# Optimization experiments

Hardware: AMD Instinct MI355X
Metric: run time of the kernel (lower is better)

## Reference

```python
import jax, jax.numpy as jnp
import numpy as np


def setup_inputs() -> dict:
    key = jax.random.key(0)
    ks = jax.random.split(key, 8)
    S, B, I, H, O = 2048, 64, 256, 512, 512
    s = 0.05  # small weight scale for numerical stability over long scans
    return {
        "x": jax.random.normal(ks[0], (S, B, I), dtype=jnp.float32),
        "Wi": jax.random.normal(ks[1], (H, I + H), dtype=jnp.float32) * s,
        "bi": jnp.zeros((H,), dtype=jnp.float32),
        "Wf": jax.random.normal(ks[2], (H, I + H), dtype=jnp.float32) * s,
        "bf": jnp.zeros((H,), dtype=jnp.float32),
        "Wg": jax.random.normal(ks[3], (H, I + H), dtype=jnp.float32) * s,
        "bg": jnp.zeros((H,), dtype=jnp.float32),
        "Wo": jax.random.normal(ks[4], (H, I + H), dtype=jnp.float32) * s,
        "bo": jnp.zeros((H,), dtype=jnp.float32),
        "Wh2o": jax.random.normal(ks[5], (O, H), dtype=jnp.float32) * s,
        "bh2o": jnp.zeros((O,), dtype=jnp.float32),
    }


def reference(x, Wi, bi, Wf, bf, Wg, bg, Wo, bo, Wh2o, bh2o):
    # x: [S, B, I] seq-major. Returns log-softmax outputs [S, B, O].
    S, B, I = x.shape
    H = Wi.shape[0]
    h0 = jnp.zeros((B, H), dtype=x.dtype)
    c0 = jnp.zeros((B, H), dtype=x.dtype)

    def step(carry, xt):
        h, c = carry
        comb = jnp.concatenate([xt, h], axis=1)  # [B, I+H]
        i = jax.nn.sigmoid(comb @ Wi.T + bi)
        f = jax.nn.sigmoid(comb @ Wf.T + bf)
        g = jnp.tanh(comb @ Wg.T + bg)
        o = jax.nn.sigmoid(comb @ Wo.T + bo)
        c_new = f * c + i * g
        h_new = o * jnp.tanh(c_new)
        out = jax.nn.log_softmax(h_new @ Wh2o.T + bh2o, axis=-1)
        return (h_new, c_new), out

    (_, _), outs = jax.lax.scan(step, (h0, c0), x)
    return outs  # [S, B, O]
```

## Files before the change

kernel.cpp:

```cpp
#include <hip/hip_runtime.h>
#include <hip/hip_bf16.h>

typedef __attribute__((ext_vector_type(8))) short bf16x8;
typedef __attribute__((ext_vector_type(4))) float f32x4;
typedef unsigned int u32t;

#define S_LEN 2048
#define BATCH 64
#define IDIM 256
#define HDIM 512
#define KDIM 768
#define ODIM 512
#define NGRP 4
#define NSLOT 32
#define LDK 792
#define FLAG_PAD 16
#define POLL_CAP 10000

#define OFF_PRE (16 * LDK * 2)
#define OFF_BIAS (OFF_PRE + 2 * 4 * 16 * 17 * 4)
#define SMEM_BYTES 98304

__device__ __forceinline__ unsigned short f2b(float f) {
  __hip_bfloat16 h = __float2bfloat16(f);
  return __builtin_bit_cast(unsigned short, h);
}
__device__ __forceinline__ float sigmoidf_(float x) { return 1.0f / (1.0f + __expf(-x)); }
__device__ __forceinline__ float tanhf_(float x) { return 1.0f - 2.0f / (1.0f + __expf(2.0f * x)); }

__device__ __forceinline__ bf16x8 cvt8(float4 v0, float4 v1) {
  bf16x8 b;
  b[0] = (short)f2b(v0.x); b[1] = (short)f2b(v0.y);
  b[2] = (short)f2b(v0.z); b[3] = (short)f2b(v0.w);
  b[4] = (short)f2b(v1.x); b[5] = (short)f2b(v1.y);
  b[6] = (short)f2b(v1.z); b[7] = (short)f2b(v1.w);
  return b;
}

__device__ __forceinline__ int l2_flag_read(int* p) {
  int z = 0;
  asm volatile("" : "+v"(z));
  return __hip_atomic_fetch_add(p, z, __ATOMIC_RELAXED, __HIP_MEMORY_SCOPE_WORKGROUP);
}

__global__ void lstm_init(const float* __restrict__ wh2o,
                          __hip_bfloat16* __restrict__ wh2o_bf,
                          __hip_bfloat16* __restrict__ h_all,
                          int* __restrict__ ctrl) {
  int idx = blockIdx.x * 256 + threadIdx.x;
  if (idx < ODIM * HDIM) wh2o_bf[idx] = __float2bfloat16(wh2o[idx]);
  if (idx < BATCH * HDIM) h_all[idx] = __float2bfloat16(0.0f);
  if (idx < 4096) ctrl[idx] = 0;
}

__global__ __launch_bounds__(512) void lstm_recur(
    const float* __restrict__ x,
    const float* __restrict__ Wi, const float* __restrict__ bi,
    const float* __restrict__ Wf, const float* __restrict__ bfp,
    const float* __restrict__ Wg, const float* __restrict__ bgp,
    const float* __restrict__ Wo, const float* __restrict__ bop,
    __hip_bfloat16* __restrict__ h_all, int* __restrict__ flags,
    int* __restrict__ cnt) {
  extern __shared__ char smem[];
  __shared__ int sel[2];
  const int tid = threadIdx.x;
  const int lane = tid & 63;
  const int wave = tid >> 6;

  if (tid == 0) {
    unsigned xcd;
    asm("s_getreg_b32 %0, hwreg(HW_REG_XCC_ID)" : "=s"(xcd));
    sel[0] = (int)(xcd & 7);
    sel[1] = atomicAdd(&cnt[(xcd & 7) * 16], 1);
  }
  __syncthreads();
  const int g = sel[0];
  const int s = sel[1];
  if (g >= NGRP || s >= NSLOT) return;

  short* comb = (short*)smem;
  float* pre = (float*)(smem + OFF_PRE);
  float* blds = (float*)(smem + OFF_BIAS);

  const int ct = wave & 3;
  const int kh = wave >> 2;
  const int rc16 = lane & 15;
  const int ksub = (lane >> 4) * 8;

  const float* wsrc = (ct == 0) ? Wi : (ct == 1) ? Wf : (ct == 2) ? Wg : Wo;
  const float* wrow = wsrc + (size_t)(s * 16 + rc16) * KDIM;
  bf16x8 bfx[4], bfh[8];
#pragma unroll
  for (int kk = 0; kk < 4; ++kk) {
    int k0 = kh * 128 + kk * 32 + ksub;
    bfx[kk] = cvt8(*(const float4*)(wrow + k0), *(const float4*)(wrow + k0 + 4));
  }
#pragma unroll
  for (int kk = 0; kk < 8; ++kk) {
    int k0 = IDIM + kh * 256 + kk * 32 + ksub;
    bfh[kk] = cvt8(*(const float4*)(wrow + k0), *(const float4*)(wrow + k0 + 4));
  }
  if (tid < 64) {
    int gate = tid >> 4;
    const float* bsrc = (gate == 0) ? bi : (gate == 1) ? bfp : (gate == 2) ? bgp : bop;
    blds[tid] = bsrc[s * 16 + (tid & 15)];
  }

  float4 rx[2];
  auto ldx = [&](int t) {
    const float4* xs = (const float4*)(x + ((size_t)t * BATCH + g * 16) * IDIM);
    rx[0] = xs[tid];
    rx[1] = xs[tid + 512];
  };
  auto stx = [&]() {
#pragma unroll
    for (int j = 0; j < 2; ++j) {
      int i = tid + j * 512;
      int r = i >> 6, k4 = i & 63;
      float4 v = rx[j];
      ushort4 u;
      u.x = f2b(v.x); u.y = f2b(v.y); u.z = f2b(v.z); u.w = f2b(v.w);
      *(ushort4*)&comb[r * LDK + k4 * 4] = u;
    }
  };

  const short* acx = &comb[rc16 * LDK + kh * 128 + ksub];
  const short* ach = &comb[rc16 * LDK + IDIM + kh * 256 + ksub];

  ldx(0);
  stx();
  __syncthreads();
  f32x4 acc = {}, acc2 = {};
  acc = __builtin_amdgcn_mfma_f32_16x16x32_bf16(*(const bf16x8*)(acx + 0), bfx[0], acc, 0, 0, 0);
  acc2 = __builtin_amdgcn_mfma_f32_16x16x32_bf16(*(const bf16x8*)(acx + 32), bfx[1], acc2, 0, 0, 0);
  acc = __builtin_amdgcn_mfma_f32_16x16x32_bf16(*(const bf16x8*)(acx + 64), bfx[2], acc, 0, 0, 0);
  acc2 = __builtin_amdgcn_mfma_f32_16x16x32_bf16(*(const bf16x8*)(acx + 96), bfx[3], acc2, 0, 0, 0);
  ldx(1);

  float cst = 0.0f;
  const int gm = tid >> 4;
  const int gn = tid & 15;
  int* myflag = flags + (g * NSLOT + s) * FLAG_PAD;
  int* gflags = flags + g * NSLOT * FLAG_PAD;

  for (int t = 0; t < S_LEN; ++t) {
    if (wave == 0) {
      for (int it = 0; it < POLL_CAP; ++it) {
        int v = (lane < NSLOT) ? l2_flag_read(gflags + lane * FLAG_PAD) : 0x7fffffff;
        if (__all(v >= t)) break;
        __builtin_amdgcn_s_sleep(1);
      }
    }
    __syncthreads();
    {
      const short* hs = (const short*)h_all + ((size_t)t * BATCH + g * 16) * HDIM;
      int r = tid >> 5, c16 = tid & 31;
      const short* sp = hs + r * HDIM + c16 * 16;
      bf16x8 v0 = *(const bf16x8*)sp;
      bf16x8 v1 = *(const bf16x8*)(sp + 8);
      short* dp = &comb[r * LDK + IDIM + c16 * 16];
      *(bf16x8*)dp = v0;
      *(bf16x8*)(dp + 8) = v1;
    }
    __syncthreads();
#pragma unroll
    for (int kk = 0; kk < 8; kk += 2) {
      acc = __builtin_amdgcn_mfma_f32_16x16x32_bf16(*(const bf16x8*)(ach + kk * 32), bfh[kk],
                                                    acc, 0, 0, 0);
      acc2 = __builtin_amdgcn_mfma_f32_16x16x32_bf16(*(const bf16x8*)(ach + kk * 32 + 32),
                                                     bfh[kk + 1], acc2, 0, 0, 0);
    }
#pragma unroll
    for (int j = 0; j < 4; ++j) {
      int m = (lane >> 4) * 4 + j;
      pre[((kh * 4 + ct) * 16 + m) * 17 + rc16] = acc[j] + acc2[j];
    }
    __syncthreads();
    if (tid < 256) {
      float pi = blds[gn] + pre[(0 * 16 + gm) * 17 + gn] + pre[(4 * 16 + gm) * 17 + gn];
      float pf = blds[16 + gn] + pre[(1 * 16 + gm) * 17 + gn] + pre[(5 * 16 + gm) * 17 + gn];
      float pg = blds[32 + gn] + pre[(2 * 16 + gm) * 17 + gn] + pre[(6 * 16 + gm) * 17 + gn];
      float po = blds[48 + gn] + pre[(3 * 16 + gm) * 17 + gn] + pre[(7 * 16 + gm) * 17 + gn];
      float ig = sigmoidf_(pi), fg = sigmoidf_(pf), gv = tanhf_(pg), og = sigmoidf_(po);
      cst = fg * cst + ig * gv;
      float hv = og * tanhf_(cst);
      float hv2 = __shfl_xor(hv, 1);
      if ((gn & 1) == 0) {
        u32t hw = (u32t)f2b(hv) | ((u32t)f2b(hv2) << 16);
        u32t* dst = (u32t*)((short*)h_all +
                            ((size_t)(t + 1) * BATCH + g * 16 + gm) * HDIM + s * 16 + gn);
        *dst = hw;
      }
    }
    asm volatile("s_waitcnt vmcnt(0)" ::: "memory");
    __syncthreads();
    if (tid == 0)
      __hip_atomic_store(myflag, t + 1, __ATOMIC_RELAXED, __HIP_MEMORY_SCOPE_WORKGROUP);
    if (t + 1 < S_LEN) {
      stx();
      __syncthreads();
      f32x4 z = {};
      acc = z;
      acc2 = z;
      acc = __builtin_amdgcn_mfma_f32_16x16x32_bf16(*(const bf16x8*)(acx + 0), bfx[0], acc, 0, 0, 0);
      acc2 = __builtin_amdgcn_mfma_f32_16x16x32_bf16(*(const bf16x8*)(acx + 32), bfx[1], acc2, 0, 0, 0);
      acc = __builtin_amdgcn_mfma_f32_16x16x32_bf16(*(const bf16x8*)(acx + 64), bfx[2], acc, 0, 0, 0);
      acc2 = __builtin_amdgcn_mfma_f32_16x16x32_bf16(*(const bf16x8*)(acx + 96), bfx[3], acc2, 0, 0, 0);
      ldx((t + 2 < S_LEN) ? t + 2 : S_LEN - 1);
    }
  }
}

__global__ __launch_bounds__(256) void lstm_out(
    const __hip_bfloat16* __restrict__ h_all,
    const __hip_bfloat16* __restrict__ wh2o_bf, const float* __restrict__ bh2o,
    float* __restrict__ out) {
  const int t = blockIdx.x;
  const int tid = threadIdx.x;
  const int lane = tid & 63;
  const int wave = tid >> 6;
  const int r0 = wave * 16;
  const short* abase = (const short*)h_all +
                       ((size_t)(t + 1) * BATCH + r0 + (lane & 15)) * HDIM + (lane >> 4) * 8;
  const short* bbase = (const short*)wh2o_bf + (size_t)(lane & 15) * HDIM + (lane >> 4) * 8;
  f32x4 acc[32];
  f32x4 zero = {0.f, 0.f, 0.f, 0.f};
#pragma unroll
  for (int n = 0; n < 32; ++n) acc[n] = zero;
  for (int kk = 0; kk < 16; ++kk) {
    bf16x8 a = *(const bf16x8*)(abase + kk * 32);
#pragma unroll
    for (int n = 0; n < 32; ++n) {
      bf16x8 b = *(const bf16x8*)(bbase + (size_t)n * 16 * HDIM + kk * 32);
      acc[n] = __builtin_amdgcn_mfma_f32_16x16x32_bf16(a, b, acc[n], 0, 0, 0);
    }
  }
  float mx[4] = {-3.0e38f, -3.0e38f, -3.0e38f, -3.0e38f};
#pragma unroll
  for (int n = 0; n < 32; ++n) {
    float bn = bh2o[n * 16 + (lane & 15)];
#pragma unroll
    for (int j = 0; j < 4; ++j) {
      acc[n][j] += bn;
      mx[j] = fmaxf(mx[j], acc[n][j]);
    }
  }
#pragma unroll
  for (int j = 0; j < 4; ++j) {
    mx[j] = fmaxf(mx[j], __shfl_xor(mx[j], 1));
    mx[j] = fmaxf(mx[j], __shfl_xor(mx[j], 2));
    mx[j] = fmaxf(mx[j], __shfl_xor(mx[j], 4));
    mx[j] = fmaxf(mx[j], __shfl_xor(mx[j], 8));
  }
  float sm[4] = {0.f, 0.f, 0.f, 0.f};
#pragma unroll
  for (int n = 0; n < 32; ++n) {
#pragma unroll
    for (int j = 0; j < 4; ++j) sm[j] += __expf(acc[n][j] - mx[j]);
  }
#pragma unroll
  for (int j = 0; j < 4; ++j) {
    sm[j] += __shfl_xor(sm[j], 1);
    sm[j] += __shfl_xor(sm[j], 2);
    sm[j] += __shfl_xor(sm[j], 4);
    sm[j] += __shfl_xor(sm[j], 8);
  }
  float ls[4];
#pragma unroll
  for (int j = 0; j < 4; ++j) ls[j] = mx[j] + __logf(sm[j]);
  float* ob = out + (size_t)t * BATCH * ODIM;
#pragma unroll
  for (int n = 0; n < 32; ++n) {
#pragma unroll
    for (int j = 0; j < 4; ++j) {
      int row = r0 + (lane >> 4) * 4 + j;
      ob[(size_t)row * ODIM + n * 16 + (lane & 15)] = acc[n][j] - ls[j];
    }
  }
}

extern "C" void kernel_launch(void* const* d_in, const int* in_sizes, int n_in,
                              void* d_out, int out_size, void* d_ws, size_t ws_size,
                              hipStream_t stream) {
  const float* x = (const float*)d_in[0];
  const float* Wi = (const float*)d_in[1];
  const float* bi = (const float*)d_in[2];
  const float* Wf = (const float*)d_in[3];
  const float* bf = (const float*)d_in[4];
  const float* Wg = (const float*)d_in[5];
  const float* bg = (const float*)d_in[6];
  const float* Wo = (const float*)d_in[7];
  const float* bo = (const float*)d_in[8];
  const float* Wh2o = (const float*)d_in[9];
  const float* bh2o = (const float*)d_in[10];

  char* ws = (char*)d_ws;
  int* cnt = (int*)ws;
  int* flags = (int*)(ws + 4096);
  __hip_bfloat16* h_all = (__hip_bfloat16*)(ws + 16384);
  size_t h_all_b = (size_t)(S_LEN + 1) * BATCH * HDIM * 2;
  __hip_bfloat16* wh2o_bf = (__hip_bfloat16*)(ws + 16384 + h_all_b);
  size_t needed = 16384 + h_all_b + (size_t)ODIM * HDIM * 2;
  if (ws_size < needed || n_in < 11) return;

  hipFuncSetAttribute((const void*)lstm_recur,
                      hipFuncAttributeMaxDynamicSharedMemorySize, SMEM_BYTES);

  lstm_init<<<1024, 256, 0, stream>>>(Wh2o, wh2o_bf, h_all, (int*)ws);
  lstm_recur<<<256, 512, SMEM_BYTES, stream>>>(x, Wi, bi, Wf, bf, Wg, bg, Wo, bo,
                                               h_all, flags, cnt);
  lstm_out<<<S_LEN, 256, 0, stream>>>(h_all, wh2o_bf, bh2o, (float*)d_out);
}
```

Before: 11.46 ms.

## Halve slots per group, use arrival-counter epoch barrier, double-buffer x slab

New measurement: 20.86 ms. 81.9% more time.

```diff
diff --git a/kernel.cpp b/kernel.cpp
--- a/kernel.cpp
+++ b/kernel.cpp
@@ -12,13 +12,16 @@
 #define KDIM 768
 #define ODIM 512
 #define NGRP 4
-#define NSLOT 32
-#define LDK 792
-#define FLAG_PAD 16
-#define POLL_CAP 10000
-
-#define OFF_PRE (16 * LDK * 2)
-#define OFF_BIAS (OFF_PRE + 2 * 4 * 16 * 17 * 4)
+#define NSLOT 16
+#define LDX 264
+#define LDH 520
+#define XSLAB (16 * LDX)
+#define EP_PAD 32
+#define POLL_CAP (1 << 16)
+
+#define OFF_H 16896
+#define OFF_PRE 33536
+#define OFF_BIAS 41984
 #define SMEM_BYTES 98304
 
 __device__ __forceinline__ unsigned short f2b(float f) {
@@ -37,7 +40,7 @@
   return b;
 }
 
-__device__ __forceinline__ int l2_flag_read(int* p) {
+__device__ __forceinline__ int l2_read(int* p) {
   int z = 0;
   asm volatile("" : "+v"(z));
   return __hip_atomic_fetch_add(p, z, __ATOMIC_RELAXED, __HIP_MEMORY_SCOPE_WORKGROUP);
@@ -50,7 +53,7 @@
   int idx = blockIdx.x * 256 + threadIdx.x;
   if (idx < ODIM * HDIM) wh2o_bf[idx] = __float2bfloat16(wh2o[idx]);
   if (idx < BATCH * HDIM) h_all[idx] = __float2bfloat16(0.0f);
-  if (idx < 4096) ctrl[idx] = 0;
+  if (idx < 16384) ctrl[idx] = 0;
 }
 
 __global__ __launch_bounds__(512) void lstm_recur(
@@ -59,8 +62,8 @@
     const float* __restrict__ Wf, const float* __restrict__ bfp,
     const float* __restrict__ Wg, const float* __restrict__ bgp,
     const float* __restrict__ Wo, const float* __restrict__ bop,
-    __hip_bfloat16* __restrict__ h_all, int* __restrict__ flags,
-    int* __restrict__ cnt) {
+    __hip_bfloat16* __restrict__ h_all, int* __restrict__ epoch,
+    int* __restrict__ stepcnt, int* __restrict__ cnt) {
   extern __shared__ char smem[];
   __shared__ int sel[2];
   const int tid = threadIdx.x;
@@ -78,32 +81,33 @@
   const int s = sel[1];
   if (g >= NGRP || s >= NSLOT) return;
 
-  short* comb = (short*)smem;
+  short* xsl = (short*)smem;
+  short* hsl = (short*)(smem + OFF_H);
   float* pre = (float*)(smem + OFF_PRE);
   float* blds = (float*)(smem + OFF_BIAS);
 
   const int ct = wave & 3;
-  const int kh = wave >> 2;
-  const int rc16 = lane & 15;
+  const int ch = wave >> 2;
+  const int a_r = lane & 15;
   const int ksub = (lane >> 4) * 8;
 
   const float* wsrc = (ct == 0) ? Wi : (ct == 1) ? Wf : (ct == 2) ? Wg : Wo;
-  const float* wrow = wsrc + (size_t)(s * 16 + rc16) * KDIM;
-  bf16x8 bfx[4], bfh[8];
-#pragma unroll
-  for (int kk = 0; kk < 4; ++kk) {
-    int k0 = kh * 128 + kk * 32 + ksub;
+  const float* wrow = wsrc + (size_t)(s * 32 + ch * 16 + a_r) * KDIM;
+  bf16x8 bfx[8], bfh[16];
+#pragma unroll
+  for (int kk = 0; kk < 8; ++kk) {
+    int k0 = kk * 32 + ksub;
     bfx[kk] = cvt8(*(const float4*)(wrow + k0), *(const float4*)(wrow + k0 + 4));
   }
 #pragma unroll
-  for (int kk = 0; kk < 8; ++kk) {
-    int k0 = IDIM + kh * 256 + kk * 32 + ksub;
+  for (int kk = 0; kk < 16; ++kk) {
+    int k0 = IDIM + kk * 32 + ksub;
     bfh[kk] = cvt8(*(const float4*)(wrow + k0), *(const float4*)(wrow + k0 + 4));
   }
-  if (tid < 64) {
-    int gate = tid >> 4;
+  if (tid < 128) {
+    int gate = tid >> 5;
     const float* bsrc = (gate == 0) ? bi : (gate == 1) ? bfp : (gate == 2) ? bgp : bop;
-    blds[tid] = bsrc[s * 16 + (tid & 15)];
+    blds[tid] = bsrc[s * 32 + (tid & 31)];
   }
 
   float4 rx[2];
@@ -112,7 +116,7 @@
     rx[0] = xs[tid];
     rx[1] = xs[tid + 512];
   };
-  auto stx = [&]() {
+  auto stx = [&](int par) {
 #pragma unroll
     for (int j = 0; j < 2; ++j) {
       int i = tid + j * 512;
@@ -120,94 +124,93 @@
       float4 v = rx[j];
       ushort4 u;
       u.x = f2b(v.x); u.y = f2b(v.y); u.z = f2b(v.z); u.w = f2b(v.w);
-      *(ushort4*)&comb[r * LDK + k4 * 4] = u;
+      *(ushort4*)&xsl[par * XSLAB + r * LDX + k4 * 4] = u;
     }
   };
 
-  const short* acx = &comb[rc16 * LDK + kh * 128 + ksub];
-  const short* ach = &comb[rc16 * LDK + IDIM + kh * 256 + ksub];
-
   ldx(0);
-  stx();
-  __syncthreads();
-  f32x4 acc = {}, acc2 = {};
-  acc = __builtin_amdgcn_mfma_f32_16x16x32_bf16(*(const bf16x8*)(acx + 0), bfx[0], acc, 0, 0, 0);
-  acc2 = __builtin_amdgcn_mfma_f32_16x16x32_bf16(*(const bf16x8*)(acx + 32), bfx[1], acc2, 0, 0, 0);
-  acc = __builtin_amdgcn_mfma_f32_16x16x32_bf16(*(const bf16x8*)(acx + 64), bfx[2], acc, 0, 0, 0);
-  acc2 = __builtin_amdgcn_mfma_f32_16x16x32_bf16(*(const bf16x8*)(acx + 96), bfx[3], acc2, 0, 0, 0);
+  stx(0);
   ldx(1);
 
   float cst = 0.0f;
-  const int gm = tid >> 4;
-  const int gn = tid & 15;
-  int* myflag = flags + (g * NSLOT + s) * FLAG_PAD;
-  int* gflags = flags + g * NSLOT * FLAG_PAD;
+  const int gr = tid >> 5;
+  const int gc = tid & 31;
+  int* myep = epoch + (g * NSLOT + s) * EP_PAD;
+  int* gep = epoch + g * NSLOT * EP_PAD;
+  int* gstep = stepcnt + g * S_LEN;
 
   for (int t = 0; t < S_LEN; ++t) {
     if (wave == 0) {
+      int old = 0;
+      if (lane == 0)
+        old = __hip_atomic_fetch_add(&gstep[t], 1, __ATOMIC_RELAXED,
+                                     __HIP_MEMORY_SCOPE_WORKGROUP);
+      old = __shfl(old, 0);
+      if (old == NSLOT - 1 && lane < NSLOT)
+        __hip_atomic_store(gep + lane * EP_PAD, t, __ATOMIC_RELAXED,
+                           __HIP_MEMORY_SCOPE_WORKGROUP);
       for (int it = 0; it < POLL_CAP; ++it) {
-        int v = (lane < NSLOT) ? l2_flag_read(gflags + lane * FLAG_PAD) : 0x7fffffff;
-        if (__all(v >= t)) break;
+        if (l2_read(myep) >= t) break;
         __builtin_amdgcn_s_sleep(1);
       }
     }
     __syncthreads();
+    stx((t + 1) & 1);
     {
       const short* hs = (const short*)h_all + ((size_t)t * BATCH + g * 16) * HDIM;
       int r = tid >> 5, c16 = tid & 31;
       const short* sp = hs + r * HDIM + c16 * 16;
       bf16x8 v0 = *(const bf16x8*)sp;
       bf16x8 v1 = *(const bf16x8*)(sp + 8);
-      short* dp = &comb[r * LDK + IDIM + c16 * 16];
+      short* dp = &hsl[r * LDH + c16 * 16];
       *(bf16x8*)dp = v0;
       *(bf16x8*)(dp + 8) = v1;
     }
+    ldx((t + 2 < S_LEN) ? t + 2 : S_LEN - 1);
     __syncthreads();
-#pragma unroll
-    for (int kk = 0; kk < 8; kk += 2) {
-      acc = __builtin_amdgcn_mfma_f32_16x16x32_bf16(*(const bf16x8*)(ach + kk * 32), bfh[kk],
-                                                    acc, 0, 0, 0);
-      acc2 = __builtin_amdgcn_mfma_f32_16x16x32_bf16(*(const bf16x8*)(ach + kk * 32 + 32),
-                                                     bfh[kk + 1], acc2, 0, 0, 0);
-    }
-#pragma unroll
-    for (int j = 0; j < 4; ++j) {
-      int m = (lane >> 4) * 4 + j;
-      pre[((kh * 4 + ct) * 16 + m) * 17 + rc16] = acc[j] + acc2[j];
+    {
+      const short* acx = &xsl[(t & 1) * XSLAB + a_r * LDX + ksub];
+      const short* ach = &hsl[a_r * LDH + ksub];
+      f32x4 c0 = {}, c1 = {}, c2 = {}, c3 = {};
+#pragma unroll
+      for (int kk = 0; kk < 8; kk += 2) {
+        c0 = __builtin_amdgcn_mfma_f32_16x16x32_bf16(*(const bf16x8*)(acx + kk * 32),
+                                                     bfx[kk], c0, 0, 0, 0);
+        c1 = __builtin_amdgcn_mfma_f32_16x16x32_bf16(*(const bf16x8*)(acx + kk * 32 + 32),
+                                                     bfx[kk + 1], c1, 0, 0, 0);
+      }
+#pragma unroll
+      for (int kk = 0; kk < 16; kk += 2) {
+        c2 = __builtin_amdgcn_mfma_f32_16x16x32_bf16(*(const bf16x8*)(ach + kk * 32),
+                                                     bfh[kk], c2, 0, 0, 0);
+        c3 = __builtin_amdgcn_mfma_f32_16x16x32_bf16(*(const bf16x8*)(ach + kk * 32 + 32),
+                                                     bfh[kk + 1], c3, 0, 0, 0);
+      }
+      const int rb = (lane >> 4) * 4;
+      const int col = ch * 16 + a_r;
+#pragma unroll
+      for (int j = 0; j < 4; ++j)
+        pre[(ct * 16 + rb + j) * 33 + col] = c0[j] + c1[j] + c2[j] + c3[j];
     }
     __syncthreads();
-    if (tid < 256) {
-      float pi = blds[gn] + pre[(0 * 16 + gm) * 17 + gn] + pre[(4 * 16 + gm) * 17 + gn];
-      float pf = blds[16 + gn] + pre[(1 * 16 + gm) * 17 + gn] + pre[(5 * 16 + gm) * 17 + gn];
-      float pg = blds[32 + gn] + pre[(2 * 16 + gm) * 17 + gn] + pre[(6 * 16 + gm) * 17 + gn];
-      float po = blds[48 + gn] + pre[(3 * 16 + gm) * 17 + gn] + pre[(7 * 16 + gm) * 17 + gn];
+    {
+      float pi = blds[gc] + pre[(0 * 16 + gr) * 33 + gc];
+      float pf = blds[32 + gc] + pre[(1 * 16 + gr) * 33 + gc];
+      float pg = blds[64 + gc] + pre[(2 * 16 + gr) * 33 + gc];
+      float po = blds[96 + gc] + pre[(3 * 16 + gr) * 33 + gc];
       float ig = sigmoidf_(pi), fg = sigmoidf_(pf), gv = tanhf_(pg), og = sigmoidf_(po);
       cst = fg * cst + ig * gv;
       float hv = og * tanhf_(cst);
       float hv2 = __shfl_xor(hv, 1);
-      if ((gn & 1) == 0) {
+      if (!(gc & 1)) {
         u32t hw = (u32t)f2b(hv) | ((u32t)f2b(hv2) << 16);
         u32t* dst = (u32t*)((short*)h_all +
-                            ((size_t)(t + 1) * BATCH + g * 16 + gm) * HDIM + s * 16 + gn);
+                            ((size_t)(t + 1) * BATCH + g * 16 + gr) * HDIM + s * 32 + gc);
         *dst = hw;
       }
     }
     asm volatile("s_waitcnt vmcnt(0)" ::: "memory");
     __syncthreads();
-    if (tid == 0)
-      __hip_atomic_store(myflag, t + 1, __ATOMIC_RELAXED, __HIP_MEMORY_SCOPE_WORKGROUP);
-    if (t + 1 < S_LEN) {
-      stx();
-      __syncthreads();
-      f32x4 z = {};
-      acc = z;
-      acc2 = z;
-      acc = __builtin_amdgcn_mfma_f32_16x16x32_bf16(*(const bf16x8*)(acx + 0), bfx[0], acc, 0, 0, 0);
-      acc2 = __builtin_amdgcn_mfma_f32_16x16x32_bf16(*(const bf16x8*)(acx + 32), bfx[1], acc2, 0, 0, 0);
-      acc = __builtin_amdgcn_mfma_f32_16x16x32_bf16(*(const bf16x8*)(acx + 64), bfx[2], acc, 0, 0, 0);
-      acc2 = __builtin_amdgcn_mfma_f32_16x16x32_bf16(*(const bf16x8*)(acx + 96), bfx[3], acc2, 0, 0, 0);
-      ldx((t + 2 < S_LEN) ? t + 2 : S_LEN - 1);
-    }
   }
 }
 
@@ -296,11 +299,12 @@
 
   char* ws = (char*)d_ws;
   int* cnt = (int*)ws;
-  int* flags = (int*)(ws + 4096);
-  __hip_bfloat16* h_all = (__hip_bfloat16*)(ws + 16384);
+  int* epoch = (int*)(ws + 2048);
+  int* stepcnt = (int*)(ws + 16384);
+  __hip_bfloat16* h_all = (__hip_bfloat16*)(ws + 65536);
   size_t h_all_b = (size_t)(S_LEN + 1) * BATCH * HDIM * 2;
-  __hip_bfloat16* wh2o_bf = (__hip_bfloat16*)(ws + 16384 + h_all_b);
-  size_t needed = 16384 + h_all_b + (size_t)ODIM * HDIM * 2;
+  __hip_bfloat16* wh2o_bf = (__hip_bfloat16*)(ws + 65536 + h_all_b);
+  size_t needed = 65536 + h_all_b + (size_t)ODIM * HDIM * 2;
   if (ws_size < needed || n_in < 11) return;
 
   hipFuncSetAttribute((const void*)lstm_recur,
@@ -308,6 +312,6 @@
 
   lstm_init<<<1024, 256, 0, stream>>>(Wh2o, wh2o_bf, h_all, (int*)ws);
   lstm_recur<<<256, 512, SMEM_BYTES, stream>>>(x, Wi, bi, Wf, bf, Wg, bg, Wo, bo,
-                                               h_all, flags, cnt);
+                                               h_all, epoch, stepcnt, cnt);
   lstm_out<<<S_LEN, 256, 0, stream>>>(h_all, wh2o_bf, bh2o, (float*)d_out);
 }
```

## Replace block barriers with LDS atomic barriers and add MFMA filler waves

Applied to the files above, without the earlier changes.

After: 12.19 ms. +6.3%, slower.

```diff
diff --git a/kernel.cpp b/kernel.cpp
--- a/kernel.cpp
+++ b/kernel.cpp
@@ -15,10 +15,11 @@
 #define NSLOT 32
 #define LDK 792
 #define FLAG_PAD 16
-#define POLL_CAP 10000
+#define POLL_CAP (1 << 16)
 
 #define OFF_PRE (16 * LDK * 2)
 #define OFF_BIAS (OFF_PRE + 2 * 4 * 16 * 17 * 4)
+#define OFF_CTL (OFF_BIAS + 256)
 #define SMEM_BYTES 98304
 
 __device__ __forceinline__ unsigned short f2b(float f) {
@@ -37,10 +38,18 @@
   return b;
 }
 
-__device__ __forceinline__ int l2_flag_read(int* p) {
+__device__ __forceinline__ int l2_read(int* p) {
   int z = 0;
   asm volatile("" : "+v"(z));
   return __hip_atomic_fetch_add(p, z, __ATOMIC_RELAXED, __HIP_MEMORY_SCOPE_WORKGROUP);
+}
+
+__device__ __forceinline__ void wbar(int* lbar, int target, int lane) {
+  asm volatile("s_waitcnt lgkmcnt(0)" ::: "memory");
+  if (lane == 0) atomicAdd(lbar, 1);
+  while (__hip_atomic_load(lbar, __ATOMIC_RELAXED, __HIP_MEMORY_SCOPE_WORKGROUP) < target) {
+  }
+  asm volatile("" ::: "memory");
 }
 
 __global__ void lstm_init(const float* __restrict__ wh2o,
@@ -50,10 +59,10 @@
   int idx = blockIdx.x * 256 + threadIdx.x;
   if (idx < ODIM * HDIM) wh2o_bf[idx] = __float2bfloat16(wh2o[idx]);
   if (idx < BATCH * HDIM) h_all[idx] = __float2bfloat16(0.0f);
-  if (idx < 4096) ctrl[idx] = 0;
-}
-
-__global__ __launch_bounds__(512) void lstm_recur(
+  if (idx < 16384) ctrl[idx] = 0;
+}
+
+__global__ __launch_bounds__(1024) void lstm_recur(
     const float* __restrict__ x,
     const float* __restrict__ Wi, const float* __restrict__ bi,
     const float* __restrict__ Wf, const float* __restrict__ bfp,
@@ -66,21 +75,42 @@
   const int tid = threadIdx.x;
   const int lane = tid & 63;
   const int wave = tid >> 6;
+  int* lbar = (int*)(smem + OFF_CTL);
+  int* ldone = (int*)(smem + OFF_CTL + 64);
 
   if (tid == 0) {
     unsigned xcd;
     asm("s_getreg_b32 %0, hwreg(HW_REG_XCC_ID)" : "=s"(xcd));
     sel[0] = (int)(xcd & 7);
     sel[1] = atomicAdd(&cnt[(xcd & 7) * 16], 1);
+    *lbar = 0;
+    *ldone = 0;
   }
   __syncthreads();
   const int g = sel[0];
   const int s = sel[1];
   if (g >= NGRP || s >= NSLOT) return;
 
+  if (wave >= 8) {
+    f32x4 acc = {};
+    bf16x8 za = {};
+    for (int it = 0; it < (1 << 18); ++it) {
+#pragma unroll
+      for (int m = 0; m < 8; ++m)
+        acc = __builtin_amdgcn_mfma_f32_16x16x32_bf16(za, za, acc, 0, 0, 0);
+      asm volatile("" : "+v"(acc));
+      if ((it & 7) == 7) {
+        if (__hip_atomic_load(ldone, __ATOMIC_RELAXED, __HIP_MEMORY_SCOPE_WORKGROUP)) break;
+      }
+    }
+    return;
+  }
+
+  __builtin_amdgcn_s_setprio(1);
   short* comb = (short*)smem;
   float* pre = (float*)(smem + OFF_PRE);
   float* blds = (float*)(smem + OFF_BIAS);
+  int bt = 0;
 
   const int ct = wave & 3;
   const int kh = wave >> 2;
@@ -129,7 +159,7 @@
 
   ldx(0);
   stx();
-  __syncthreads();
+  bt += 8; wbar(lbar, bt, lane);
   f32x4 acc = {}, acc2 = {};
   acc = __builtin_amdgcn_mfma_f32_16x16x32_bf16(*(const bf16x8*)(acx + 0), bfx[0], acc, 0, 0, 0);
   acc2 = __builtin_amdgcn_mfma_f32_16x16x32_bf16(*(const bf16x8*)(acx + 32), bfx[1], acc2, 0, 0, 0);
@@ -146,12 +176,12 @@
   for (int t = 0; t < S_LEN; ++t) {
     if (wave == 0) {
       for (int it = 0; it < POLL_CAP; ++it) {
-        int v = (lane < NSLOT) ? l2_flag_read(gflags + lane * FLAG_PAD) : 0x7fffffff;
+        int v = (lane < NSLOT) ? l2_read(gflags + lane * FLAG_PAD) : 0x7fffffff;
         if (__all(v >= t)) break;
         __builtin_amdgcn_s_sleep(1);
       }
     }
-    __syncthreads();
+    bt += 8; wbar(lbar, bt, lane);
     {
       const short* hs = (const short*)h_all + ((size_t)t * BATCH + g * 16) * HDIM;
       int r = tid >> 5, c16 = tid & 31;
@@ -162,7 +192,7 @@
       *(bf16x8*)dp = v0;
       *(bf16x8*)(dp + 8) = v1;
     }
-    __syncthreads();
+    bt += 8; wbar(lbar, bt, lane);
 #pragma unroll
     for (int kk = 0; kk < 8; kk += 2) {
       acc = __builtin_amdgcn_mfma_f32_16x16x32_bf16(*(const bf16x8*)(ach + kk * 32), bfh[kk],
@@ -175,7 +205,7 @@
       int m = (lane >> 4) * 4 + j;
       pre[((kh * 4 + ct) * 16 + m) * 17 + rc16] = acc[j] + acc2[j];
     }
-    __syncthreads();
+    bt += 8; wbar(lbar, bt, lane);
     if (tid < 256) {
       float pi = blds[gn] + pre[(0 * 16 + gm) * 17 + gn] + pre[(4 * 16 + gm) * 17 + gn];
       float pf = blds[16 + gn] + pre[(1 * 16 + gm) * 17 + gn] + pre[(5 * 16 + gm) * 17 + gn];
@@ -193,12 +223,12 @@
       }
     }
     asm volatile("s_waitcnt vmcnt(0)" ::: "memory");
-    __syncthreads();
+    bt += 8; wbar(lbar, bt, lane);
     if (tid == 0)
       __hip_atomic_store(myflag, t + 1, __ATOMIC_RELAXED, __HIP_MEMORY_SCOPE_WORKGROUP);
     if (t + 1 < S_LEN) {
       stx();
-      __syncthreads();
+      bt += 8; wbar(lbar, bt, lane);
       f32x4 z = {};
       acc = z;
       acc2 = z;
@@ -209,6 +239,8 @@
       ldx((t + 2 < S_LEN) ? t + 2 : S_LEN - 1);
     }
   }
+  if (tid == 0)
+    __hip_atomic_store(ldone, 1, __ATOMIC_RELAXED, __HIP_MEMORY_SCOPE_WORKGROUP);
 }
 
 __global__ __launch_bounds__(256) void lstm_out(
@@ -297,17 +329,17 @@
   char* ws = (char*)d_ws;
   int* cnt = (int*)ws;
   int* flags = (int*)(ws + 4096);
-  __hip_bfloat16* h_all = (__hip_bfloat16*)(ws + 16384);
+  __hip_bfloat16* h_all = (__hip_bfloat16*)(ws + 65536);
   size_t h_all_b = (size_t)(S_LEN + 1) * BATCH * HDIM * 2;
-  __hip_bfloat16* wh2o_bf = (__hip_bfloat16*)(ws + 16384 + h_all_b);
-  size_t needed = 16384 + h_all_b + (size_t)ODIM * HDIM * 2;
+  __hip_bfloat16* wh2o_bf = (__hip_bfloat16*)(ws + 65536 + h_all_b);
+  size_t needed = 65536 + h_all_b + (size_t)ODIM * HDIM * 2;
   if (ws_size < needed || n_in < 11) return;
 
   hipFuncSetAttribute((const void*)lstm_recur,
                       hipFuncAttributeMaxDynamicSharedMemorySize, SMEM_BYTES);
 
   lstm_init<<<1024, 256, 0, stream>>>(Wh2o, wh2o_bf, h_all, (int*)ws);
-  lstm_recur<<<256, 512, SMEM_BYTES, stream>>>(x, Wi, bi, Wf, bf, Wg, bg, Wo, bo,
-                                               h_all, flags, cnt);
+  lstm_recur<<<256, 1024, SMEM_BYTES, stream>>>(x, Wi, bi, Wf, bf, Wg, bg, Wo, bo,
+                                                h_all, flags, cnt);
   lstm_out<<<S_LEN, 256, 0, stream>>>(h_all, wh2o_bf, bh2o, (float*)d_out);
 }
```
